# Performance work log

Hardware: AMD Instinct MI355X
Metric: run time of the kernel (lower is better)

Reference implementation:

```python
import jax, jax.numpy as jnp
import numpy as np


def conv2d_same(x, w, b=None):
    # x: [B,C,H,W], w: [O,I,kh,kw] (OIHW), SAME padding, stride 1
    y = jax.lax.conv_general_dilated(
        x, w, window_strides=(1, 1), padding="SAME",
        dimension_numbers=("NCHW", "OIHW", "NCHW"))
    if b is not None:
        y = y + b[None, :, None, None]
    return y


def setup_inputs() -> dict:
    key = jax.random.key(0)
    ks = jax.random.split(key, 20)
    B, Cin, Ce, Ci, Cout, H, W, K = 16, 32, 32, 32, 32, 128, 128, 3
    WSCALE = 0.1  # keep tanh in its non-saturated range
    inp = {
        "x": jax.random.normal(ks[0], (B, Cin, H, W), jnp.float32),
        "h_e": jax.random.normal(ks[1], (B, Ce, H, W), jnp.float32),
        "h_i": jax.random.normal(ks[2], (B, Ci, H, W), jnp.float32),
        "W_in_e": jax.random.normal(ks[3], (Ce, Cin, K, K), jnp.float32) * WSCALE,
        "b_in_e": jax.random.normal(ks[4], (Ce,), jnp.float32) * WSCALE,
        "W_in_i": jax.random.normal(ks[5], (Ci, Cin, K, K), jnp.float32) * WSCALE,
        "b_in_i": jax.random.normal(ks[6], (Ci,), jnp.float32) * WSCALE,
        "W_e_e": jax.random.normal(ks[7], (Ce, Ce, K, K), jnp.float32) * WSCALE,
        "b_e_e": jax.random.normal(ks[8], (Ce,), jnp.float32) * WSCALE,
        "W_e_i": jax.random.normal(ks[9], (Ci, Ce, K, K), jnp.float32) * WSCALE,
        "b_e_i": jax.random.normal(ks[10], (Ci,), jnp.float32) * WSCALE,
        "W_e_out": jax.random.normal(ks[11], (Cout, Ce, K, K), jnp.float32) * WSCALE,
        "b_e_out": jax.random.normal(ks[12], (Cout,), jnp.float32) * WSCALE,
        "W_i_e": jax.random.normal(ks[13], (Ce, Ci, K, K), jnp.float32) * WSCALE,
        "b_i_e": jax.random.normal(ks[14], (Ce,), jnp.float32) * WSCALE,
        "W_i_i": jax.random.normal(ks[15], (Ci, Ci, K, K), jnp.float32) * WSCALE,
        "b_i_i": jax.random.normal(ks[16], (Ci,), jnp.float32) * WSCALE,
        "tau_e": jnp.ones((Ce,), jnp.float32),
        "tau_i": jnp.ones((Ci,), jnp.float32),
    }
    return inp


def reference(x, h_e, h_i,
              W_in_e, b_in_e, W_in_i, b_in_i,
              W_e_e, b_e_e, W_e_i, b_e_i, W_e_out, b_e_out,
              W_i_e, b_i_e, W_i_i, b_i_i,
              tau_e, tau_i):
    # Per-cell-type conv message passing with Dale's-law rectified kernels:
    # excitatory (E) sources add, inhibitory (I) sources subtract; rectified
    # convs clamp weight/bias to be non-negative (Conv2dRectify -> relu).
    relu = jax.nn.relu
    cand_e = (conv2d_same(x, W_in_e, b_in_e)
              + conv2d_same(h_e, relu(W_e_e), relu(b_e_e))
              - conv2d_same(h_i, relu(W_i_e), relu(b_i_e)))
    cand_i = (conv2d_same(x, W_in_i, b_in_i)
              + conv2d_same(h_e, relu(W_e_i), relu(b_e_i))
              - conv2d_same(h_i, relu(W_i_i), relu(b_i_i)))
    # cell nonlinearity (Tanh)
    cand_e = jnp.tanh(cand_e)
    cand_i = jnp.tanh(cand_i)
    # tau-based leaky integration, per-channel time constants (tau >= 1)
    inv_te = 1.0 / jnp.maximum(tau_e, 1.0)[None, :, None, None]
    inv_ti = 1.0 / jnp.maximum(tau_i, 1.0)[None, :, None, None]
    h_e_new = (1.0 - inv_te) * h_e + inv_te * cand_e
    h_i_new = (1.0 - inv_ti) * h_i + inv_ti * cand_i
    # output population: rectified conv from the excitatory state
    out = jnp.tanh(conv2d_same(h_e_new, relu(W_e_out), relu(b_e_out)))
    return out, h_e_new, h_i_new
```

## Files before the change

kernel.cpp:

```cpp
#include <hip/hip_runtime.h>
#include <math.h>

#define BB 16
#define C  32
#define H  128
#define W  128

#define HE_OFF   ((size_t)BB*C*H*W)
#define HI_OFF   ((size_t)2*BB*C*H*W)

#define WSB_WA    0
#define WSB_WO    110592
#define WSB_BIAS  129024
#define WSB_ITAU  129280
#define WSB_BOUT  129536

typedef _Float16 half8 __attribute__((ext_vector_type(8)));
typedef float    f32x4 __attribute__((ext_vector_type(4)));

__device__ __forceinline__ float fast_tanh(float x) {
  float ax = fabsf(x);
  float e  = __expf(2.f * ax);
  float t  = 1.f - 2.f / (e + 1.f);
  return copysignf(t, x);
}

__global__ void prep_kernel(const float* __restrict__ W_in_e, const float* __restrict__ b_in_e,
                            const float* __restrict__ W_in_i, const float* __restrict__ b_in_i,
                            const float* __restrict__ W_e_e,  const float* __restrict__ b_e_e,
                            const float* __restrict__ W_e_i,  const float* __restrict__ b_e_i,
                            const float* __restrict__ W_e_out,const float* __restrict__ b_e_out,
                            const float* __restrict__ W_i_e,  const float* __restrict__ b_i_e,
                            const float* __restrict__ W_i_i,  const float* __restrict__ b_i_i,
                            const float* __restrict__ tau_e,  const float* __restrict__ tau_i,
                            unsigned char* __restrict__ ws) {
  int t = blockIdx.x * 256 + threadIdx.x;
  _Float16* wa = (_Float16*)(ws + WSB_WA);
  _Float16* wo = (_Float16*)(ws + WSB_WO);
  float* bias64 = (float*)(ws + WSB_BIAS);
  float* itau64 = (float*)(ws + WSB_ITAU);
  float* bout   = (float*)(ws + WSB_BOUT);

  if (t < 55296) {
    int s = t / 18432, r1 = t % 18432;
    int tap = r1 / 2048, r2 = r1 % 2048;
    int mt = r2 / 512, r3 = r2 % 512;
    int lane = r3 >> 3, j = r3 & 7;
    int ch64 = mt*16 + (lane & 15);
    int cin  = (lane >> 4)*8 + j;
    int dy = tap / 3, dx = tap % 3;
    float v;
    if (ch64 < C) {
      int off = ((ch64*C + cin)*3 + dy)*3 + dx;
      v = (s==0) ? W_in_e[off] : (s==1) ? fmaxf(W_e_e[off],0.f) : -fmaxf(W_i_e[off],0.f);
    } else {
      int off = (((ch64-C)*C + cin)*3 + dy)*3 + dx;
      v = (s==0) ? W_in_i[off] : (s==1) ? fmaxf(W_e_i[off],0.f) : -fmaxf(W_i_i[off],0.f);
    }
    wa[t] = (_Float16)v;
  }
  if (t < 9216) {
    int tap = t / 1024, r2 = t % 1024;
    int mt = r2 / 512, r3 = r2 % 512;
    int lane = r3 >> 3, j = r3 & 7;
    int ch  = mt*16 + (lane & 15);
    int cin = (lane >> 4)*8 + j;
    int dy = tap / 3, dx = tap % 3;
    wo[t] = (_Float16)fmaxf(W_e_out[((ch*C + cin)*3 + dy)*3 + dx], 0.f);
  }
  if (t < 64) {
    if (t < 32) {
      bias64[t] = b_in_e[t] + fmaxf(b_e_e[t],0.f) - fmaxf(b_i_e[t],0.f);
      itau64[t] = 1.f / fmaxf(tau_e[t], 1.f);
      bout[t]   = fmaxf(b_e_out[t], 0.f);
    } else {
      bias64[t] = b_in_i[t-32] + fmaxf(b_e_i[t-32],0.f) - fmaxf(b_i_i[t-32],0.f);
      itau64[t] = 1.f / fmaxf(tau_i[t-32], 1.f);
    }
  }
}

__global__ __launch_bounds__(256) void cell_kernel(
    const float* __restrict__ x, const float* __restrict__ h_e, const float* __restrict__ h_i,
    const unsigned char* __restrict__ ws, float* __restrict__ out) {
  __shared__ f32x4 smem[3600];
  _Float16* tile = (_Float16*)smem;
  f32x4*    wlds = smem + 1296;

  const int b   = blockIdx.z;
  const int ty0 = blockIdx.y * 16, tx0 = blockIdx.x * 16;
  const int tid = threadIdx.x;
  const int wid = tid >> 6, l = tid & 63;
  const int q   = l >> 4, xl = l & 15;

  const float* bias64 = (const float*)(ws + WSB_BIAS);
  const float* itau64 = (const float*)(ws + WSB_ITAU);

  f32x4 acc[4][4];
  #pragma unroll
  for (int mt = 0; mt < 4; ++mt) {
    f32x4 bv = *(const f32x4*)(bias64 + mt*16 + q*4);
    #pragma unroll
    for (int nt = 0; nt < 4; ++nt) acc[mt][nt] = bv;
  }

  for (int s = 0; s < 3; ++s) {
    const float* src = (s==0 ? x : (s==1 ? h_e : h_i)) + (size_t)b*C*H*W;
    __syncthreads();
    for (int i = tid; i < 10368; i += 256) {
      int c = i / 324, rem = i % 324;
      int yy = rem / 18, xx = rem % 18;
      int gr = ty0 - 1 + yy, gc = tx0 - 1 + xx;
      float v = ((unsigned)gr < H && (unsigned)gc < W) ? src[(c*H + gr)*W + gc] : 0.f;
      int baddr = yy*1152 + xx*64 + (((c>>3) ^ ((xx>>1)&3)) << 4) + ((c&7) << 1);
      tile[baddr >> 1] = (_Float16)v;
    }
    const f32x4* wsrc = (const f32x4*)(ws + WSB_WA) + s*2304;
    #pragma unroll
    for (int k2 = 0; k2 < 9; ++k2) wlds[k2*256 + tid] = wsrc[k2*256 + tid];
    __syncthreads();

    #pragma unroll
    for (int dy = 0; dy < 3; ++dy) {
      #pragma unroll
      for (int dx = 0; dx < 3; ++dx) {
        const int tap  = dy*3 + dx;
        const int xcol = xl + dx;
        const int swz  = (q ^ ((xcol>>1)&3)) << 4;
        half8 bf[4];
        #pragma unroll
        for (int nt = 0; nt < 4; ++nt) {
          int yrow = wid*4 + nt + dy;
          bf[nt] = *(const half8*)((const char*)tile + yrow*1152 + xcol*64 + swz);
        }
        #pragma unroll
        for (int mt = 0; mt < 4; ++mt) {
          half8 af = *(const half8*)((const char*)wlds + ((tap*4 + mt)*64 + l)*16);
          #pragma unroll
          for (int nt = 0; nt < 4; ++nt)
            acc[mt][nt] = __builtin_amdgcn_mfma_f32_16x16x32_f16(af, bf[nt], acc[mt][nt], 0, 0, 0);
        }
      }
    }
  }

  #pragma unroll
  for (int mt = 0; mt < 4; ++mt) {
    f32x4 tv = *(const f32x4*)(itau64 + mt*16 + q*4);
    const float* hsrc = (mt < 2) ? h_e : h_i;
    float*       dst  = out + ((mt < 2) ? HE_OFF : HI_OFF);
    #pragma unroll
    for (int nt = 0; nt < 4; ++nt) {
      int pix = wid*64 + nt*16 + xl;
      int gy = ty0 + (pix >> 4), gx = tx0 + (pix & 15);
      #pragma unroll
      for (int r = 0; r < 4; ++r) {
        int ch = (mt*16 + q*4 + r) & 31;
        size_t idx = (((size_t)b*C + ch)*H + gy)*W + gx;
        float it = tv[r];
        dst[idx] = (1.f - it)*hsrc[idx] + it*fast_tanh(acc[mt][nt][r]);
      }
    }
  }
}

__global__ __launch_bounds__(256) void out_kernel(
    const unsigned char* __restrict__ ws, float* __restrict__ out) {
  __shared__ f32x4 smem[2448];
  _Float16* tile = (_Float16*)smem;
  f32x4*    wlds = smem + 1296;

  const int b   = blockIdx.z;
  const int ty0 = blockIdx.y * 16, tx0 = blockIdx.x * 16;
  const int tid = threadIdx.x;
  const int wid = tid >> 6, l = tid & 63;
  const int q   = l >> 4, xl = l & 15;

  const float* bout = (const float*)(ws + WSB_BOUT);
  const float* src  = out + HE_OFF + (size_t)b*C*H*W;

  f32x4 acc[2][4];
  #pragma unroll
  for (int mt = 0; mt < 2; ++mt) {
    f32x4 bv = *(const f32x4*)(bout + mt*16 + q*4);
    #pragma unroll
    for (int nt = 0; nt < 4; ++nt) acc[mt][nt] = bv;
  }

  for (int i = tid; i < 10368; i += 256) {
    int c = i / 324, rem = i % 324;
    int yy = rem / 18, xx = rem % 18;
    int gr = ty0 - 1 + yy, gc = tx0 - 1 + xx;
    float v = ((unsigned)gr < H && (unsigned)gc < W) ? src[(c*H + gr)*W + gc] : 0.f;
    int baddr = yy*1152 + xx*64 + (((c>>3) ^ ((xx>>1)&3)) << 4) + ((c&7) << 1);
    tile[baddr >> 1] = (_Float16)v;
  }
  const f32x4* wsrc = (const f32x4*)(ws + WSB_WO);
  #pragma unroll
  for (int k2 = 0; k2 < 5; ++k2) {
    int off = k2*256 + tid;
    if (off < 1152) wlds[off] = wsrc[off];
  }
  __syncthreads();

  #pragma unroll
  for (int dy = 0; dy < 3; ++dy) {
    #pragma unroll
    for (int dx = 0; dx < 3; ++dx) {
      const int tap  = dy*3 + dx;
      const int xcol = xl + dx;
      const int swz  = (q ^ ((xcol>>1)&3)) << 4;
      half8 bf[4];
      #pragma unroll
      for (int nt = 0; nt < 4; ++nt) {
        int yrow = wid*4 + nt + dy;
        bf[nt] = *(const half8*)((const char*)tile + yrow*1152 + xcol*64 + swz);
      }
      #pragma unroll
      for (int mt = 0; mt < 2; ++mt) {
        half8 af = *(const half8*)((const char*)wlds + ((tap*2 + mt)*64 + l)*16);
        #pragma unroll
        for (int nt = 0; nt < 4; ++nt)
          acc[mt][nt] = __builtin_amdgcn_mfma_f32_16x16x32_f16(af, bf[nt], acc[mt][nt], 0, 0, 0);
      }
    }
  }

  #pragma unroll
  for (int mt = 0; mt < 2; ++mt) {
    #pragma unroll
    for (int nt = 0; nt < 4; ++nt) {
      int pix = wid*64 + nt*16 + xl;
      int gy = ty0 + (pix >> 4), gx = tx0 + (pix & 15);
      #pragma unroll
      for (int r = 0; r < 4; ++r) {
        int ch = mt*16 + q*4 + r;
        out[(((size_t)b*C + ch)*H + gy)*W + gx] = fast_tanh(acc[mt][nt][r]);
      }
    }
  }
}

extern "C" void kernel_launch(void* const* d_in, const int* in_sizes, int n_in,
                              void* d_out, int out_size, void* d_ws, size_t ws_size,
                              hipStream_t stream) {
  const float* x      = (const float*)d_in[0];
  const float* h_e    = (const float*)d_in[1];
  const float* h_i    = (const float*)d_in[2];
  const float* W_in_e = (const float*)d_in[3];
  const float* b_in_e = (const float*)d_in[4];
  const float* W_in_i = (const float*)d_in[5];
  const float* b_in_i = (const float*)d_in[6];
  const float* W_e_e  = (const float*)d_in[7];
  const float* b_e_e  = (const float*)d_in[8];
  const float* W_e_i  = (const float*)d_in[9];
  const float* b_e_i  = (const float*)d_in[10];
  const float* W_e_out= (const float*)d_in[11];
  const float* b_e_out= (const float*)d_in[12];
  const float* W_i_e  = (const float*)d_in[13];
  const float* b_i_e  = (const float*)d_in[14];
  const float* W_i_i  = (const float*)d_in[15];
  const float* b_i_i  = (const float*)d_in[16];
  const float* tau_e  = (const float*)d_in[17];
  const float* tau_i  = (const float*)d_in[18];

  unsigned char* ws = (unsigned char*)d_ws;
  float* out = (float*)d_out;

  prep_kernel<<<216, 256, 0, stream>>>(W_in_e, b_in_e, W_in_i, b_in_i,
                                       W_e_e, b_e_e, W_e_i, b_e_i,
                                       W_e_out, b_e_out, W_i_e, b_i_e,
                                       W_i_i, b_i_i, tau_e, tau_i, ws);

  dim3 grid(W/16, H/16, BB);
  cell_kernel<<<grid, 256, 0, stream>>>(x, h_e, h_i, ws, out);
  out_kernel<<<grid, 256, 0, stream>>>(ws, out);
}
```

Baseline: 378.2 us.

## Pre-convert inputs to channel-last fp16 workspace and stream per-source halo tiles

```diff
diff --git a/kernel.cpp b/kernel.cpp
--- a/kernel.cpp
+++ b/kernel.cpp
@@ -14,8 +14,13 @@
 #define WSB_BIAS  129024
 #define WSB_ITAU  129280
 #define WSB_BOUT  129536
+#define WSB_F16   131072
+#define TBYTES    16777216
+#define IMGB      1048576
+#define WS_NEED   (WSB_F16 + 4*(size_t)TBYTES)
 
 typedef _Float16 half8 __attribute__((ext_vector_type(8)));
+typedef _Float16 half4 __attribute__((ext_vector_type(4)));
 typedef float    f32x4 __attribute__((ext_vector_type(4)));
 
 __device__ __forceinline__ float fast_tanh(float x) {
@@ -80,7 +85,190 @@
   }
 }
 
-__global__ __launch_bounds__(256) void cell_kernel(
+__global__ __launch_bounds__(128) void convert_kernel(
+    const float* __restrict__ x, const float* __restrict__ he,
+    const float* __restrict__ hi, unsigned char* __restrict__ ws) {
+  const int bid = blockIdx.x;
+  const int b = bid >> 7, y = bid & 127;
+  const int lane = threadIdx.x;
+  const float* srcs[3] = {x, he, hi};
+  #pragma unroll
+  for (int t = 0; t < 3; ++t) {
+    const float* src = srcs[t] + (size_t)b*C*H*W + (size_t)y*W + lane;
+    _Float16* dst = (_Float16*)(ws + WSB_F16 + (size_t)t*TBYTES)
+                    + (size_t)b*(C*H*W) + ((size_t)y*W + lane)*C;
+    half8 o[4];
+    #pragma unroll
+    for (int c = 0; c < 32; ++c)
+      o[c>>3][c&7] = (_Float16)src[(size_t)c*H*W];
+    #pragma unroll
+    for (int k = 0; k < 4; ++k) *((half8*)dst + k) = o[k];
+  }
+}
+
+__global__ __launch_bounds__(256, 4) void cell_kernel(
+    const unsigned char* __restrict__ ws, float* __restrict__ out) {
+  __shared__ _Float16 tile[10368];
+
+  const int b   = blockIdx.z;
+  const int ty0 = blockIdx.y * 16, tx0 = blockIdx.x * 16;
+  const int tid = threadIdx.x;
+  const int wid = tid >> 6, l = tid & 63;
+  const int q   = l >> 4, xl = l & 15;
+
+  const float* bias64 = (const float*)(ws + WSB_BIAS);
+  const float* itau64 = (const float*)(ws + WSB_ITAU);
+
+  f32x4 acc[4][4];
+  #pragma unroll
+  for (int mt = 0; mt < 4; ++mt) {
+    f32x4 bv = *(const f32x4*)(bias64 + mt*16 + q*4);
+    #pragma unroll
+    for (int nt = 0; nt < 4; ++nt) acc[mt][nt] = bv;
+  }
+
+  for (int s = 0; s < 3; ++s) {
+    const unsigned char* src16 = ws + WSB_F16 + (size_t)s*TBYTES + (size_t)b*IMGB;
+    __syncthreads();
+    for (int i = tid; i < 1296; i += 256) {
+      int yy = i / 72, r = i % 72;
+      int xx = r >> 2, k = r & 3;
+      int gr = ty0 - 1 + yy, gc = tx0 - 1 + xx;
+      half8 v;
+      #pragma unroll
+      for (int j = 0; j < 8; ++j) v[j] = (_Float16)0.f;
+      if ((unsigned)gr < H && (unsigned)gc < W)
+        v = *(const half8*)(src16 + (gr*W + gc)*64 + k*16);
+      *(half8*)((char*)tile + yy*1152 + xx*64 + ((k ^ ((xx>>1)&3)) << 4)) = v;
+    }
+    __syncthreads();
+
+    const unsigned char* wsrc = ws + WSB_WA + s*36864;
+    #pragma unroll
+    for (int dy = 0; dy < 3; ++dy) {
+      #pragma unroll
+      for (int dx = 0; dx < 3; ++dx) {
+        const int tap  = dy*3 + dx;
+        const int xcol = xl + dx;
+        const int swz  = (q ^ ((xcol>>1)&3)) << 4;
+        half8 bf[4];
+        #pragma unroll
+        for (int nt = 0; nt < 4; ++nt) {
+          int yrow = wid*4 + nt + dy;
+          bf[nt] = *(const half8*)((const char*)tile + yrow*1152 + xcol*64 + swz);
+        }
+        #pragma unroll
+        for (int mt = 0; mt < 4; ++mt) {
+          half8 af = *(const half8*)(wsrc + ((tap*4 + mt)*64 + l)*16);
+          #pragma unroll
+          for (int nt = 0; nt < 4; ++nt)
+            acc[mt][nt] = __builtin_amdgcn_mfma_f32_16x16x32_f16(af, bf[nt], acc[mt][nt], 0, 0, 0);
+        }
+      }
+    }
+  }
+
+  #pragma unroll
+  for (int mt = 0; mt < 4; ++mt) {
+    f32x4 tv = *(const f32x4*)(itau64 + mt*16 + q*4);
+    const unsigned char* h16 = ws + WSB_F16 + (size_t)((mt < 2) ? 1 : 2)*TBYTES + (size_t)b*IMGB;
+    unsigned char*     hen16 = (unsigned char*)ws + WSB_F16 + (size_t)3*TBYTES + (size_t)b*IMGB;
+    float*             dst32 = out + ((mt < 2) ? HE_OFF : HI_OFF);
+    const int chbase = (mt & 1)*16 + q*4;
+    #pragma unroll
+    for (int nt = 0; nt < 4; ++nt) {
+      int pix = wid*64 + nt*16 + xl;
+      int gy = ty0 + (pix >> 4), gx = tx0 + (pix & 15);
+      int pixb = (gy*W + gx)*64;
+      half4 hv = *(const half4*)(h16 + pixb + chbase*2);
+      half4 h16out;
+      #pragma unroll
+      for (int r = 0; r < 4; ++r) {
+        int ch = chbase + r;
+        float it = tv[r];
+        float res = (1.f - it)*(float)hv[r] + it*fast_tanh(acc[mt][nt][r]);
+        dst32[(((size_t)b*C + ch)*H + gy)*W + gx] = res;
+        h16out[r] = (_Float16)res;
+      }
+      if (mt < 2) *(half4*)(hen16 + pixb + chbase*2) = h16out;
+    }
+  }
+}
+
+__global__ __launch_bounds__(256, 4) void out_kernel(
+    const unsigned char* __restrict__ ws, float* __restrict__ out) {
+  __shared__ _Float16 tile[10368];
+
+  const int b   = blockIdx.z;
+  const int ty0 = blockIdx.y * 16, tx0 = blockIdx.x * 16;
+  const int tid = threadIdx.x;
+  const int wid = tid >> 6, l = tid & 63;
+  const int q   = l >> 4, xl = l & 15;
+
+  const float* bout = (const float*)(ws + WSB_BOUT);
+  const unsigned char* src16 = ws + WSB_F16 + (size_t)3*TBYTES + (size_t)b*IMGB;
+
+  f32x4 acc[2][4];
+  #pragma unroll
+  for (int mt = 0; mt < 2; ++mt) {
+    f32x4 bv = *(const f32x4*)(bout + mt*16 + q*4);
+    #pragma unroll
+    for (int nt = 0; nt < 4; ++nt) acc[mt][nt] = bv;
+  }
+
+  for (int i = tid; i < 1296; i += 256) {
+    int yy = i / 72, r = i % 72;
+    int xx = r >> 2, k = r & 3;
+    int gr = ty0 - 1 + yy, gc = tx0 - 1 + xx;
+    half8 v;
+    #pragma unroll
+    for (int j = 0; j < 8; ++j) v[j] = (_Float16)0.f;
+    if ((unsigned)gr < H && (unsigned)gc < W)
+      v = *(const half8*)(src16 + (gr*W + gc)*64 + k*16);
+    *(half8*)((char*)tile + yy*1152 + xx*64 + ((k ^ ((xx>>1)&3)) << 4)) = v;
+  }
+  __syncthreads();
+
+  const unsigned char* wsrc = ws + WSB_WO;
+  #pragma unroll
+  for (int dy = 0; dy < 3; ++dy) {
+    #pragma unroll
+    for (int dx = 0; dx < 3; ++dx) {
+      const int tap  = dy*3 + dx;
+      const int xcol = xl + dx;
+      const int swz  = (q ^ ((xcol>>1)&3)) << 4;
+      half8 bf[4];
+      #pragma unroll
+      for (int nt = 0; nt < 4; ++nt) {
+        int yrow = wid*4 + nt + dy;
+        bf[nt] = *(const half8*)((const char*)tile + yrow*1152 + xcol*64 + swz);
+      }
+      #pragma unroll
+      for (int mt = 0; mt < 2; ++mt) {
+        half8 af = *(const half8*)(wsrc + ((tap*2 + mt)*64 + l)*16);
+        #pragma unroll
+        for (int nt = 0; nt < 4; ++nt)
+          acc[mt][nt] = __builtin_amdgcn_mfma_f32_16x16x32_f16(af, bf[nt], acc[mt][nt], 0, 0, 0);
+      }
+    }
+  }
+
+  #pragma unroll
+  for (int mt = 0; mt < 2; ++mt) {
+    #pragma unroll
+    for (int nt = 0; nt < 4; ++nt) {
+      int pix = wid*64 + nt*16 + xl;
+      int gy = ty0 + (pix >> 4), gx = tx0 + (pix & 15);
+      #pragma unroll
+      for (int r = 0; r < 4; ++r) {
+        int ch = mt*16 + q*4 + r;
+        out[(((size_t)b*C + ch)*H + gy)*W + gx] = fast_tanh(acc[mt][nt][r]);
+      }
+    }
+  }
+}
+
+__global__ __launch_bounds__(256) void cell_kernel_fb(
     const float* __restrict__ x, const float* __restrict__ h_e, const float* __restrict__ h_i,
     const unsigned char* __restrict__ ws, float* __restrict__ out) {
   __shared__ f32x4 smem[3600];
@@ -164,7 +352,7 @@
   }
 }
 
-__global__ __launch_bounds__(256) void out_kernel(
+__global__ __launch_bounds__(256) void out_kernel_fb(
     const unsigned char* __restrict__ ws, float* __restrict__ out) {
   __shared__ f32x4 smem[2448];
   _Float16* tile = (_Float16*)smem;
@@ -273,6 +461,13 @@
                                        W_i_i, b_i_i, tau_e, tau_i, ws);
 
   dim3 grid(W/16, H/16, BB);
-  cell_kernel<<<grid, 256, 0, stream>>>(x, h_e, h_i, ws, out);
-  out_kernel<<<grid, 256, 0, stream>>>(ws, out);
-}
+
+  if (ws_size >= WS_NEED) {
+    convert_kernel<<<BB*H, 128, 0, stream>>>(x, h_e, h_i, ws);
+    cell_kernel<<<grid, 256, 0, stream>>>(ws, out);
+    out_kernel<<<grid, 256, 0, stream>>>(ws, out);
+  } else {
+    cell_kernel_fb<<<grid, 256, 0, stream>>>(x, h_e, h_i, ws, out);
+    out_kernel_fb<<<grid, 256, 0, stream>>>(ws, out);
+  }
+}
```

After: 314.4 us. 16.9% less time.

## Fuse cell and output convs with halo recompute and pre-converted fp16 NHWC inputs

Applied to the files above, without the earlier changes.

```diff
diff --git a/kernel.cpp b/kernel.cpp
--- a/kernel.cpp
+++ b/kernel.cpp
@@ -14,8 +14,12 @@
 #define WSB_BIAS  129024
 #define WSB_ITAU  129280
 #define WSB_BOUT  129536
+#define WSB_F16   131072
+#define TBYTES    16777216
+#define IMGB      1048576
 
 typedef _Float16 half8 __attribute__((ext_vector_type(8)));
+typedef _Float16 half4 __attribute__((ext_vector_type(4)));
 typedef float    f32x4 __attribute__((ext_vector_type(4)));
 
 __device__ __forceinline__ float fast_tanh(float x) {
@@ -80,12 +84,69 @@
   }
 }
 
-__global__ __launch_bounds__(256) void cell_kernel(
-    const float* __restrict__ x, const float* __restrict__ h_e, const float* __restrict__ h_i,
+__global__ __launch_bounds__(128) void convert_kernel(
+    const float* __restrict__ x, const float* __restrict__ he,
+    const float* __restrict__ hi, unsigned char* __restrict__ ws) {
+  const int bid = blockIdx.x;
+  const int b = bid >> 7, y = bid & 127;
+  const int lane = threadIdx.x;
+  const float* srcs[3] = {x, he, hi};
+  #pragma unroll
+  for (int t = 0; t < 3; ++t) {
+    const float* src = srcs[t] + (size_t)b*C*H*W + (size_t)y*W + lane;
+    _Float16* dst = (_Float16*)(ws + WSB_F16 + (size_t)t*TBYTES)
+                    + (size_t)b*(C*H*W) + ((size_t)y*W + lane)*C;
+    half8 o[4];
+    #pragma unroll
+    for (int c = 0; c < 32; ++c)
+      o[c>>3][c&7] = (_Float16)src[(size_t)c*H*W];
+    #pragma unroll
+    for (int k = 0; k < 4; ++k) *((half8*)dst + k) = o[k];
+  }
+}
+
+__device__ __forceinline__ void stage20(const unsigned char* __restrict__ src,
+                                        _Float16* buf, int ty0, int tx0, int tid) {
+  for (int i = tid; i < 1600; i += 256) {
+    int yy = i / 80, rem = i % 80;
+    int xx = rem >> 2, k = rem & 3;
+    int gr = ty0 - 2 + yy, gc = tx0 - 2 + xx;
+    half8 v;
+    #pragma unroll
+    for (int j = 0; j < 8; ++j) v[j] = (_Float16)0.f;
+    if ((unsigned)gr < H && (unsigned)gc < W)
+      v = *(const half8*)(src + (gr*W + gc)*64 + k*16);
+    *(half8*)((char*)buf + (yy*20 + xx)*64 + ((k ^ ((xx>>1)&3)) << 4)) = v;
+  }
+}
+
+#define CAND_MFMA(BUFP, WPTR) do {                                            \
+  _Pragma("unroll") for (int dy = 0; dy < 3; ++dy) {                          \
+    _Pragma("unroll") for (int dx = 0; dx < 3; ++dx) {                        \
+      const int tap = dy*3 + dx;                                              \
+      half8 bf[6];                                                            \
+      _Pragma("unroll") for (int nt = 0; nt < 6; ++nt) {                      \
+        if (nt < NTE) {                                                       \
+          int rr = pr[nt] + dy, cc = pc[nt] + dx;                             \
+          bf[nt] = *(const half8*)((const char*)(BUFP) + (rr*20 + cc)*64      \
+                                   + ((q ^ ((cc>>1)&3)) << 4));               \
+        }                                                                     \
+      }                                                                       \
+      _Pragma("unroll") for (int mt = 0; mt < 4; ++mt) {                      \
+        half8 af = *(const half8*)((WPTR) + ((tap*4 + mt)*64 + l)*16);        \
+        _Pragma("unroll") for (int nt = 0; nt < 6; ++nt)                      \
+          if (nt < NTE)                                                       \
+            acc[mt][nt] = __builtin_amdgcn_mfma_f32_16x16x32_f16(             \
+                af, bf[nt], acc[mt][nt], 0, 0, 0);                            \
+      }                                                                       \
+    }                                                                         \
+  }                                                                           \
+} while (0)
+
+__global__ __launch_bounds__(256, 2) void fused_kernel(
     const unsigned char* __restrict__ ws, float* __restrict__ out) {
-  __shared__ f32x4 smem[3600];
-  _Float16* tile = (_Float16*)smem;
-  f32x4*    wlds = smem + 1296;
+  __shared__ _Float16 buf0[12800];
+  __shared__ _Float16 buf1[12800];
 
   const int b   = blockIdx.z;
   const int ty0 = blockIdx.y * 16, tx0 = blockIdx.x * 16;
@@ -93,149 +154,121 @@
   const int wid = tid >> 6, l = tid & 63;
   const int q   = l >> 4, xl = l & 15;
 
+  int pr[6], pc[6];
+  #pragma unroll
+  for (int nt = 0; nt < 6; ++nt) {
+    int px = (nt*4 + wid)*16 + xl;
+    int v  = px < 324 ? px : 323;
+    pr[nt] = v / 18;
+    pc[nt] = v - pr[nt]*18;
+  }
+  const int NTE = (wid == 0) ? 6 : 5;
+
   const float* bias64 = (const float*)(ws + WSB_BIAS);
   const float* itau64 = (const float*)(ws + WSB_ITAU);
 
-  f32x4 acc[4][4];
+  f32x4 acc[4][6];
   #pragma unroll
   for (int mt = 0; mt < 4; ++mt) {
     f32x4 bv = *(const f32x4*)(bias64 + mt*16 + q*4);
     #pragma unroll
-    for (int nt = 0; nt < 4; ++nt) acc[mt][nt] = bv;
-  }
-
-  for (int s = 0; s < 3; ++s) {
-    const float* src = (s==0 ? x : (s==1 ? h_e : h_i)) + (size_t)b*C*H*W;
-    __syncthreads();
-    for (int i = tid; i < 10368; i += 256) {
-      int c = i / 324, rem = i % 324;
-      int yy = rem / 18, xx = rem % 18;
-      int gr = ty0 - 1 + yy, gc = tx0 - 1 + xx;
-      float v = ((unsigned)gr < H && (unsigned)gc < W) ? src[(c*H + gr)*W + gc] : 0.f;
-      int baddr = yy*1152 + xx*64 + (((c>>3) ^ ((xx>>1)&3)) << 4) + ((c&7) << 1);
-      tile[baddr >> 1] = (_Float16)v;
-    }
-    const f32x4* wsrc = (const f32x4*)(ws + WSB_WA) + s*2304;
-    #pragma unroll
-    for (int k2 = 0; k2 < 9; ++k2) wlds[k2*256 + tid] = wsrc[k2*256 + tid];
-    __syncthreads();
-
-    #pragma unroll
-    for (int dy = 0; dy < 3; ++dy) {
-      #pragma unroll
-      for (int dx = 0; dx < 3; ++dx) {
-        const int tap  = dy*3 + dx;
-        const int xcol = xl + dx;
-        const int swz  = (q ^ ((xcol>>1)&3)) << 4;
-        half8 bf[4];
+    for (int nt = 0; nt < 6; ++nt) acc[mt][nt] = bv;
+  }
+
+  const unsigned char* t16 = ws + WSB_F16 + (size_t)b*IMGB;
+  stage20(t16 + 0*(size_t)TBYTES, buf0, ty0, tx0, tid);
+  stage20(t16 + 1*(size_t)TBYTES, buf1, ty0, tx0, tid);
+  __syncthreads();
+  CAND_MFMA(buf0, ws + WSB_WA + 0*36864);
+  CAND_MFMA(buf1, ws + WSB_WA + 1*36864);
+  __syncthreads();
+  stage20(t16 + 2*(size_t)TBYTES, buf0, ty0, tx0, tid);
+  __syncthreads();
+  CAND_MFMA(buf0, ws + WSB_WA + 2*36864);
+
+  #pragma unroll
+  for (int mt = 0; mt < 4; ++mt) {
+    f32x4 tv = *(const f32x4*)(itau64 + mt*16 + q*4);
+    const int chb  = (mt & 1)*16 + q*4;
+    const int klog = (mt & 1)*2 + (q >> 1);
+    _Float16* hbuf = (mt < 2) ? buf1 : buf0;
+    float* dst32 = out + ((mt < 2) ? HE_OFF : HI_OFF);
+    #pragma unroll
+    for (int nt = 0; nt < 6; ++nt) {
+      if (nt < NTE) {
+        int px = (nt*4 + wid)*16 + xl;
+        bool pxv = px < 324;
+        int r = pr[nt], c = pc[nt];
+        int gy = ty0 - 1 + r, gx = tx0 - 1 + c;
+        bool inimg = ((unsigned)gy < H) && ((unsigned)gx < W);
+        bool interior = (r >= 1) && (r < 17) && (c >= 1) && (c < 17);
+        int slot  = ((r + 1)*20 + (c + 1))*64;
+        int kphys = klog ^ (((c + 1) >> 1) & 3);
+        half4 hold = *(const half4*)((const char*)hbuf + slot + kphys*16 + (q & 1)*8);
+        float res[4];
         #pragma unroll
-        for (int nt = 0; nt < 4; ++nt) {
-          int yrow = wid*4 + nt + dy;
-          bf[nt] = *(const half8*)((const char*)tile + yrow*1152 + xcol*64 + swz);
+        for (int rr = 0; rr < 4; ++rr) {
+          float it = tv[rr];
+          res[rr] = (1.f - it)*(float)hold[rr] + it*fast_tanh(acc[mt][nt][rr]);
         }
-        #pragma unroll
-        for (int mt = 0; mt < 4; ++mt) {
-          half8 af = *(const half8*)((const char*)wlds + ((tap*4 + mt)*64 + l)*16);
+        if (mt < 2 && pxv) {
+          half4 h16;
           #pragma unroll
-          for (int nt = 0; nt < 4; ++nt)
-            acc[mt][nt] = __builtin_amdgcn_mfma_f32_16x16x32_f16(af, bf[nt], acc[mt][nt], 0, 0, 0);
+          for (int rr = 0; rr < 4; ++rr)
+            h16[rr] = inimg ? (_Float16)res[rr] : (_Float16)0.f;
+          *(half4*)((char*)buf1 + slot + kphys*16 + (q & 1)*8) = h16;
+        }
+        if (pxv && interior) {
+          #pragma unroll
+          for (int rr = 0; rr < 4; ++rr)
+            dst32[(((size_t)b*C + (chb + rr))*H + gy)*W + gx] = res[rr];
         }
       }
     }
   }
-
-  #pragma unroll
-  for (int mt = 0; mt < 4; ++mt) {
-    f32x4 tv = *(const f32x4*)(itau64 + mt*16 + q*4);
-    const float* hsrc = (mt < 2) ? h_e : h_i;
-    float*       dst  = out + ((mt < 2) ? HE_OFF : HI_OFF);
-    #pragma unroll
-    for (int nt = 0; nt < 4; ++nt) {
-      int pix = wid*64 + nt*16 + xl;
-      int gy = ty0 + (pix >> 4), gx = tx0 + (pix & 15);
-      #pragma unroll
-      for (int r = 0; r < 4; ++r) {
-        int ch = (mt*16 + q*4 + r) & 31;
-        size_t idx = (((size_t)b*C + ch)*H + gy)*W + gx;
-        float it = tv[r];
-        dst[idx] = (1.f - it)*hsrc[idx] + it*fast_tanh(acc[mt][nt][r]);
-      }
-    }
-  }
-}
-
-__global__ __launch_bounds__(256) void out_kernel(
-    const unsigned char* __restrict__ ws, float* __restrict__ out) {
-  __shared__ f32x4 smem[2448];
-  _Float16* tile = (_Float16*)smem;
-  f32x4*    wlds = smem + 1296;
-
-  const int b   = blockIdx.z;
-  const int ty0 = blockIdx.y * 16, tx0 = blockIdx.x * 16;
-  const int tid = threadIdx.x;
-  const int wid = tid >> 6, l = tid & 63;
-  const int q   = l >> 4, xl = l & 15;
-
+  __syncthreads();
+
+  const unsigned char* wo = ws + WSB_WO;
   const float* bout = (const float*)(ws + WSB_BOUT);
-  const float* src  = out + HE_OFF + (size_t)b*C*H*W;
-
-  f32x4 acc[2][4];
+  f32x4 ao[2][4];
   #pragma unroll
   for (int mt = 0; mt < 2; ++mt) {
     f32x4 bv = *(const f32x4*)(bout + mt*16 + q*4);
     #pragma unroll
-    for (int nt = 0; nt < 4; ++nt) acc[mt][nt] = bv;
-  }
-
-  for (int i = tid; i < 10368; i += 256) {
-    int c = i / 324, rem = i % 324;
-    int yy = rem / 18, xx = rem % 18;
-    int gr = ty0 - 1 + yy, gc = tx0 - 1 + xx;
-    float v = ((unsigned)gr < H && (unsigned)gc < W) ? src[(c*H + gr)*W + gc] : 0.f;
-    int baddr = yy*1152 + xx*64 + (((c>>3) ^ ((xx>>1)&3)) << 4) + ((c&7) << 1);
-    tile[baddr >> 1] = (_Float16)v;
-  }
-  const f32x4* wsrc = (const f32x4*)(ws + WSB_WO);
-  #pragma unroll
-  for (int k2 = 0; k2 < 5; ++k2) {
-    int off = k2*256 + tid;
-    if (off < 1152) wlds[off] = wsrc[off];
-  }
-  __syncthreads();
-
+    for (int nt = 0; nt < 4; ++nt) ao[mt][nt] = bv;
+  }
   #pragma unroll
   for (int dy = 0; dy < 3; ++dy) {
     #pragma unroll
     for (int dx = 0; dx < 3; ++dx) {
-      const int tap  = dy*3 + dx;
-      const int xcol = xl + dx;
-      const int swz  = (q ^ ((xcol>>1)&3)) << 4;
+      const int tap = dy*3 + dx;
       half8 bf[4];
       #pragma unroll
       for (int nt = 0; nt < 4; ++nt) {
-        int yrow = wid*4 + nt + dy;
-        bf[nt] = *(const half8*)((const char*)tile + yrow*1152 + xcol*64 + swz);
+        int px = (nt*4 + wid)*16 + xl;
+        int ti = (px >> 4) + dy + 1, tj = (px & 15) + dx + 1;
+        bf[nt] = *(const half8*)((const char*)buf1 + (ti*20 + tj)*64
+                                 + ((q ^ ((tj>>1)&3)) << 4));
       }
       #pragma unroll
       for (int mt = 0; mt < 2; ++mt) {
-        half8 af = *(const half8*)((const char*)wlds + ((tap*2 + mt)*64 + l)*16);
+        half8 af = *(const half8*)(wo + ((tap*2 + mt)*64 + l)*16);
         #pragma unroll
         for (int nt = 0; nt < 4; ++nt)
-          acc[mt][nt] = __builtin_amdgcn_mfma_f32_16x16x32_f16(af, bf[nt], acc[mt][nt], 0, 0, 0);
+          ao[mt][nt] = __builtin_amdgcn_mfma_f32_16x16x32_f16(af, bf[nt], ao[mt][nt], 0, 0, 0);
       }
     }
   }
-
   #pragma unroll
   for (int mt = 0; mt < 2; ++mt) {
     #pragma unroll
     for (int nt = 0; nt < 4; ++nt) {
-      int pix = wid*64 + nt*16 + xl;
-      int gy = ty0 + (pix >> 4), gx = tx0 + (pix & 15);
+      int px = (nt*4 + wid)*16 + xl;
+      int gy = ty0 + (px >> 4), gx = tx0 + (px & 15);
       #pragma unroll
-      for (int r = 0; r < 4; ++r) {
-        int ch = mt*16 + q*4 + r;
-        out[(((size_t)b*C + ch)*H + gy)*W + gx] = fast_tanh(acc[mt][nt][r]);
+      for (int rr = 0; rr < 4; ++rr) {
+        int ch = mt*16 + q*4 + rr;
+        out[(((size_t)b*C + ch)*H + gy)*W + gx] = fast_tanh(ao[mt][nt][rr]);
       }
     }
   }
@@ -272,7 +305,8 @@
                                        W_e_out, b_e_out, W_i_e, b_i_e,
                                        W_i_i, b_i_i, tau_e, tau_i, ws);
 
+  convert_kernel<<<BB*H, 128, 0, stream>>>(x, h_e, h_i, ws);
+
   dim3 grid(W/16, H/16, BB);
-  cell_kernel<<<grid, 256, 0, stream>>>(x, h_e, h_i, ws, out);
-  out_kernel<<<grid, 256, 0, stream>>>(ws, out);
-}
+  fused_kernel<<<grid, 256, 0, stream>>>(ws, out);
+}
```

New measurement: 358.1 us. -5.3%, faster.
